# Kernel optimization log

Measured on AMD Instinct MI355X. Metric: run time of the kernel, lower is better.

The kernel has to match this reference:

```python
import jax, jax.numpy as jnp
import numpy as np

TOP_K = 2
ALPHA = 1.702
LIMIT = 7.0


def setup_inputs() -> dict:
    key = jax.random.key(0)
    ks = jax.random.split(key, 7)
    B, S, H, I, E = 1, 2048, 1024, 1024, 8
    scale = 0.02
    return {
        "hidden_states": jax.random.normal(ks[0], (B, S, H), dtype=jnp.float32),
        "router_w": jax.random.normal(ks[1], (H, E), dtype=jnp.float32) * scale,
        "router_b": jax.random.normal(ks[2], (E,), dtype=jnp.float32) * scale,
        "gate_up_proj": jax.random.normal(ks[3], (E, H, 2 * I), dtype=jnp.float32) * scale,
        "gate_up_bias": jax.random.normal(ks[4], (E, 2 * I), dtype=jnp.float32) * scale,
        "down_proj": jax.random.normal(ks[5], (E, I, H), dtype=jnp.float32) * scale,
        "down_bias": jax.random.normal(ks[6], (E, H), dtype=jnp.float32) * scale,
    }


def reference(hidden_states, router_w, router_b, gate_up_proj, gate_up_bias, down_proj, down_bias):
    # hidden_states: [B, S, H]; gate_up_proj: [E, H, 2I]; down_proj: [E, I, H]
    E = gate_up_proj.shape[0]
    # --- router (GPT-OSS style): top-k logits, softmax over top-k, scatter to E slots ---
    logits = jnp.einsum("bsh,he->bse", hidden_states, router_w) + router_b  # [B,S,E]
    top_vals, top_idx = jax.lax.top_k(logits, TOP_K)                         # [B,S,K]
    topk_weights = jax.nn.softmax(top_vals, axis=-1)                         # [B,S,K]
    onehot = jax.nn.one_hot(top_idx, E, dtype=logits.dtype)                  # [B,S,K,E]
    router_scores = jnp.einsum("bsk,bske->bse", topk_weights, onehot)        # [B,S,E]
    # --- expert compute (dense over the small expert axis; selection via gather below,
    #     which matches the sparsity-masked grouped matmul + all_to_all_combine math) ---
    gu = jnp.einsum("bsh,ehf->bsef", hidden_states, gate_up_proj) + gate_up_bias  # [B,S,E,2I]
    gate = gu[..., 0::2]  # interleaved gate
    up = gu[..., 1::2]    # interleaved up
    gate = jnp.minimum(gate, LIMIT)
    up = jnp.maximum(jnp.minimum(up, LIMIT), -LIMIT)
    glu = gate * jax.nn.sigmoid(gate * ALPHA)
    activated = (up + 1.0) * glu                                             # [B,S,E,I]
    down = jnp.einsum("bsei,eih->bseh", activated, down_proj) + down_bias    # [B,S,E,H]
    # combine: gather each token's K selected expert outputs, weighted sum
    sel = jnp.take_along_axis(down, top_idx[..., None], axis=2)              # [B,S,K,H]
    output = jnp.einsum("bskh,bsk->bsh", sel, topk_weights)                  # [B,S,H]
    return output, router_scores
```

## Files before the change

kernel.cpp:

```cpp
#include <hip/hip_runtime.h>
#include <stdint.h>


#define Sd 2048
#define Hd 1024
#define Id 1024

typedef __bf16 bf16x8 __attribute__((ext_vector_type(8)));
typedef _Float16 f16x8 __attribute__((ext_vector_type(8)));
typedef float f32x4 __attribute__((ext_vector_type(4)));

__device__ __forceinline__ f32x4 mfma_bf16(bf16x8 a, bf16x8 b, f32x4 c) {
  return __builtin_amdgcn_mfma_f32_16x16x32_bf16(a, b, c, 0, 0, 0);
}

__device__ __forceinline__ void gload16(const __bf16* g, __bf16* l) {
  __builtin_amdgcn_global_load_lds(
      (const __attribute__((address_space(1))) unsigned int*)g,
      (__attribute__((address_space(3))) unsigned int*)l, 16, 0, 0);
}

__device__ __forceinline__ unsigned int packbf(float lo, float hi) {
  __bf16 a = (__bf16)lo, b = (__bf16)hi;
  return (unsigned int)__builtin_bit_cast(unsigned short, a) |
         ((unsigned int)__builtin_bit_cast(unsigned short, b) << 16);
}

__global__ __launch_bounds__(256) void k_router(
    const float* __restrict__ x, const float* __restrict__ rw,
    const float* __restrict__ rb, float* __restrict__ scores,
    float* __restrict__ topw, int* __restrict__ eid,
    __bf16* __restrict__ xb) {
  const int lane = threadIdx.x & 63;
  const int t = blockIdx.x * 4 + (threadIdx.x >> 6);
  float acc[8];
#pragma unroll
  for (int e = 0; e < 8; ++e) acc[e] = 0.f;
  const float* xr = x + (size_t)t * Hd;
  unsigned int* xbo = (unsigned int*)(xb + (size_t)t * Hd);
#pragma unroll
  for (int j = 0; j < 8; ++j) {
    int h = j * 128 + lane * 2;
    float2 xv = *(const float2*)(xr + h);
    xbo[h >> 1] = packbf(xv.x, xv.y);
    const float4* wp = (const float4*)(rw + h * 8);
    float4 a0 = wp[0], a1 = wp[1], b0 = wp[2], b1 = wp[3];
    acc[0] += xv.x * a0.x; acc[1] += xv.x * a0.y;
    acc[2] += xv.x * a0.z; acc[3] += xv.x * a0.w;
    acc[4] += xv.x * a1.x; acc[5] += xv.x * a1.y;
    acc[6] += xv.x * a1.z; acc[7] += xv.x * a1.w;
    acc[0] += xv.y * b0.x; acc[1] += xv.y * b0.y;
    acc[2] += xv.y * b0.z; acc[3] += xv.y * b0.w;
    acc[4] += xv.y * b1.x; acc[5] += xv.y * b1.y;
    acc[6] += xv.y * b1.z; acc[7] += xv.y * b1.w;
  }
#pragma unroll
  for (int m = 32; m >= 1; m >>= 1) {
#pragma unroll
    for (int e = 0; e < 8; ++e) acc[e] += __shfl_xor(acc[e], m, 64);
  }
  if (lane == 0) {
    float lg[8];
#pragma unroll
    for (int e = 0; e < 8; ++e) lg[e] = acc[e] + rb[e];
    int i0 = 0; float v0 = lg[0];
#pragma unroll
    for (int e = 1; e < 8; ++e) if (lg[e] > v0) { v0 = lg[e]; i0 = e; }
    int i1 = -1; float v1 = -3.4e38f;
#pragma unroll
    for (int e = 0; e < 8; ++e) if (e != i0 && lg[e] > v1) { v1 = lg[e]; i1 = e; }
    float e1 = __expf(v1 - v0);
    float s = 1.f + e1;
    float w0 = 1.f / s, w1v = e1 / s;
#pragma unroll
    for (int e = 0; e < 8; ++e)
      scores[t * 8 + e] = (e == i0) ? w0 : ((e == i1) ? w1v : 0.f);
    topw[t * 2] = w0;
    topw[t * 2 + 1] = w1v;
    eid[t] = i0 | (i1 << 4);
  }
}

__global__ __launch_bounds__(256) void k_assign(
    const int* __restrict__ eid, int* __restrict__ cnt,
    int* __restrict__ assign, int* __restrict__ tokmap) {
  __shared__ int lcnt[8];
  const int tid = threadIdx.x;
  if (tid < 8) lcnt[tid] = 0;
  __syncthreads();
  for (int t = tid; t < 2048; t += 256) {
    int v = eid[t];
    int i0 = v & 15, i1 = v >> 4;
    int s0 = atomicAdd(&lcnt[i0], 1);
    assign[i0 * 2048 + s0] = t * 2;
    tokmap[t * 2] = (i0 << 11) | s0;
    int s1 = atomicAdd(&lcnt[i1], 1);
    assign[i1 * 2048 + s1] = t * 2 + 1;
    tokmap[t * 2 + 1] = (i1 << 11) | s1;
  }
  __syncthreads();
  if (tid < 8) cnt[tid] = lcnt[tid];
}

__global__ __launch_bounds__(256) void k_gather(
    const __bf16* __restrict__ xb, const int* __restrict__ cnt,
    const int* __restrict__ assign, __bf16* __restrict__ xg) {
  const int u = blockIdx.x;
  int acc = 0, myE = -1, myU0 = 0, nE = 0;
#pragma unroll
  for (int q = 0; q < 8; ++q) {
    int units = ((cnt[q] + 255) >> 8) * 16;
    if (u >= acc && u < acc + units) { myE = q; myU0 = acc; nE = cnt[q]; }
    acc += units;
  }
  if (myE < 0) return;
  const int lane = threadIdx.x & 63;
  const int wv = threadIdx.x >> 6;
  const int row = lane & 15, koff = (lane >> 4) * 8;
  const int slot = (u - myU0) * 16 + row;
  const bool valid = slot < nE;
  int tok = 0;
  if (valid) tok = assign[myE * 2048 + slot] >> 1;
  const __bf16* src = xb + (size_t)tok * Hd + koff;
#pragma unroll
  for (int s = 0; s < 8; ++s) {
    int k32 = wv + 4 * s;
    bf16x8 v;
#pragma unroll
    for (int j = 0; j < 8; ++j) v[j] = (__bf16)0.f;
    if (valid) v = *(const bf16x8*)(src + k32 * 32);
    *(bf16x8*)(xg + (((size_t)u * 32 + k32) * 64 + lane) * 8) = v;
  }
}

__global__ __launch_bounds__(256) void k_pre1(const float* __restrict__ wgu,
                                              __bf16* __restrict__ w1f) {
  const int b = blockIdx.x;
  const int nt = b & 7, kt = (b >> 3) & 15, e = b >> 7;
  __shared__ unsigned int Ls[16][16][34];
  const int tid = threadIdx.x;
  const int w = tid >> 6, lane = tid & 63;
  const float* src = wgu + (size_t)e * (1024 * 2048) +
                     (size_t)(kt * 64 + w * 16) * 2048 + nt * 256;
  const int i0 = lane * 2;
  const int c0 = i0 & 15, u0 = (i0 >> 4) * 2;
  const int c1 = (i0 + 1) & 15, u1 = ((i0 + 1) >> 4) * 2;
#pragma unroll
  for (int rp = 0; rp < 8; ++rp) {
    float4 fa = *(const float4*)(src + (size_t)(rp * 2) * 2048 + lane * 4);
    float4 fb = *(const float4*)(src + (size_t)(rp * 2 + 1) * 2048 + lane * 4);
    int r = w * 8 + rp;
    Ls[u0][c0][r] = packbf(fa.x, fb.x);
    Ls[u0 + 1][c0][r] = packbf(fa.y, fb.y);
    Ls[u1][c1][r] = packbf(fa.z, fb.z);
    Ls[u1 + 1][c1][r] = packbf(fa.w, fb.w);
  }
  __syncthreads();
  const int khi = lane >> 4, c = lane & 15;
#pragma unroll
  for (int uu = 0; uu < 8; ++uu) {
    int ul = w * 8 + uu, vu = ul >> 1, k32l = ul & 1;
    const unsigned int* p = &Ls[vu][c][k32l * 16 + khi * 4];
    uint2 q0 = *(const uint2*)p;
    uint2 q1 = *(const uint2*)(p + 2);
    int itg = nt * 8 + (vu >> 1), vf = vu & 1;
    size_t row = ((size_t)(e * 64 + itg) * 2 + vf) * 32 + (kt * 2 + k32l);
    uint4 o = {q0.x, q0.y, q1.x, q1.y};
    *(uint4*)(w1f + row * 512 + lane * 8) = o;
  }
}

__global__ __launch_bounds__(256) void k_pre2(const float* __restrict__ wdn,
                                              __bf16* __restrict__ w2f) {
  const int b = blockIdx.x;
  const int nt = b & 3, kt = (b >> 2) & 15, e = b >> 6;
  __shared__ unsigned int Ls[16][16][34];
  const int tid = threadIdx.x;
  const int w = tid >> 6, lane = tid & 63;
  const float* src = wdn + (size_t)e * (1024 * 1024) +
                     (size_t)(kt * 64 + w * 16) * 1024 + nt * 256;
#pragma unroll
  for (int rp = 0; rp < 8; ++rp) {
    float4 fa = *(const float4*)(src + (size_t)(rp * 2) * 1024 + lane * 4);
    float4 fb = *(const float4*)(src + (size_t)(rp * 2 + 1) * 1024 + lane * 4);
    int r = w * 8 + rp;
    float va[4] = {fa.x, fa.y, fa.z, fa.w};
    float vb[4] = {fb.x, fb.y, fb.z, fb.w};
#pragma unroll
    for (int q = 0; q < 4; ++q) {
      int cl = lane * 4 + q;
      Ls[cl >> 4][cl & 15][r] = packbf(va[q], vb[q]);
    }
  }
  __syncthreads();
  const int khi = lane >> 4, c = lane & 15;
#pragma unroll
  for (int uu = 0; uu < 8; ++uu) {
    int ul = w * 8 + uu, Fl = ul >> 1, k32l = ul & 1;
    const unsigned int* p = &Ls[Fl][c][k32l * 16 + khi * 4];
    uint2 q0 = *(const uint2*)p;
    uint2 q1 = *(const uint2*)(p + 2);
    size_t row = (size_t)(e * 64 + nt * 16 + Fl) * 32 + (kt * 2 + k32l);
    uint4 o = {q0.x, q0.y, q1.x, q1.y};
    *(uint4*)(w2f + row * 512 + lane * 8) = o;
  }
}

__global__ __launch_bounds__(512, 2) void k_gemm1(
    const __bf16* __restrict__ xg, const __bf16* __restrict__ w1f,
    const float* __restrict__ gub, const int* __restrict__ cnt,
    __bf16* __restrict__ abuf) {
  const int e = blockIdx.x & 7;
  const int r = blockIdx.x >> 3;
  const int it = r & 31;
  const int ms = r >> 5;
  const int n = cnt[e];
  if (n <= 0) return;
  __shared__ __align__(16) __bf16 Bs[4][32][512];
  __shared__ __align__(16) __bf16 Ts[256][48];
  const int tid = threadIdx.x;
  const int lane = tid & 63;
  const int wv = tid >> 6;

#pragma unroll
  for (int s = 0; s < 16; ++s) {
    int idx = s * 512 + tid;
    int v = idx >> 11, k = (idx >> 6) & 31, l = idx & 63;
    size_t rowv = (size_t)(e * 64 + it * 2 + (v >> 1)) * 2 + (v & 1);
    gload16(w1f + (rowv * 32 + k) * 512 + l * 8, &Bs[v][k][l * 8]);
  }
  float bgv[2], buv[2];
#pragma unroll
  for (int p = 0; p < 2; ++p) {
    const int col = it * 32 + p * 16 + (lane & 15);
    bgv[p] = gub[e * 2048 + 2 * col];
    buv[p] = gub[e * 2048 + 2 * col + 1];
  }
  int eb = 0;
#pragma unroll
  for (int q = 0; q < 8; ++q) eb += (q < e) ? (((cnt[q] + 255) >> 8) << 8) : 0;
  const int u0 = eb >> 4;
  const int nmt = (n + 255) >> 8;

  for (int mt = ms; mt < nmt; mt += 2) {
    __syncthreads();
    const __bf16* ap0 =
        xg + ((size_t)(u0 + mt * 16 + 2 * wv) * 32) * 512 + lane * 8;
    const __bf16* ap1 = ap0 + (size_t)32 * 512;
    f32x4 acc[2][4];
#pragma unroll
    for (int a = 0; a < 2; ++a)
#pragma unroll
      for (int b = 0; b < 4; ++b) acc[a][b] = (f32x4){0.f, 0.f, 0.f, 0.f};
    bf16x8 pf[4][2];
#pragma unroll
    for (int d = 0; d < 4; ++d) {
      pf[d][0] = *(const bf16x8*)(ap0 + d * 512);
      pf[d][1] = *(const bf16x8*)(ap1 + d * 512);
    }
#pragma unroll 4
    for (int ks = 0; ks < 28; ++ks) {
      bf16x8 b[4];
#pragma unroll
      for (int v = 0; v < 4; ++v) b[v] = *(const bf16x8*)&Bs[v][ks][lane * 8];
#pragma unroll
      for (int v = 0; v < 4; ++v) {
        acc[0][v] = mfma_bf16(pf[ks & 3][0], b[v], acc[0][v]);
        acc[1][v] = mfma_bf16(pf[ks & 3][1], b[v], acc[1][v]);
      }
      pf[ks & 3][0] = *(const bf16x8*)(ap0 + (ks + 4) * 512);
      pf[ks & 3][1] = *(const bf16x8*)(ap1 + (ks + 4) * 512);
    }
#pragma unroll
    for (int ks = 28; ks < 32; ++ks) {
      bf16x8 b[4];
#pragma unroll
      for (int v = 0; v < 4; ++v) b[v] = *(const bf16x8*)&Bs[v][ks][lane * 8];
#pragma unroll
      for (int v = 0; v < 4; ++v) {
        acc[0][v] = mfma_bf16(pf[ks & 3][0], b[v], acc[0][v]);
        acc[1][v] = mfma_bf16(pf[ks & 3][1], b[v], acc[1][v]);
      }
    }
#pragma unroll
    for (int itgl = 0; itgl < 2; ++itgl) {
      const int colL = itgl * 16 + (lane & 15);
#pragma unroll
      for (int mi = 0; mi < 2; ++mi) {
        f32x4 ag = acc[mi][itgl * 2];
        f32x4 au = acc[mi][itgl * 2 + 1];
#pragma unroll
        for (int rr = 0; rr < 4; ++rr) {
          int row = wv * 32 + mi * 16 + (lane >> 4) * 4 + rr;
          float g = fminf(ag[rr] + bgv[itgl], 7.f);
          float u = fminf(fmaxf(au[rr] + buv[itgl], -7.f), 7.f);
          float sg = 1.f / (1.f + __expf(-1.702f * g));
          Ts[row][colL] = (__bf16)((u + 1.f) * (g * sg));
        }
      }
    }
    __syncthreads();
#pragma unroll
    for (int h2 = 0; h2 < 2; ++h2) {
      int idx = h2 * 512 + tid;
      int sbl = idx >> 6, l = idx & 63;
      bf16x8 v = *(const bf16x8*)&Ts[sbl * 16 + (l & 15)][(l >> 4) * 8];
      size_t o = ((size_t)(u0 + mt * 16 + sbl) * 32 + it) * 512 + l * 8;
      *(bf16x8*)(abuf + o) = v;
    }
  }
}

__global__ __launch_bounds__(512, 2) void k_gemm2(
    const __bf16* __restrict__ abuf, const __bf16* __restrict__ w2f,
    const float* __restrict__ dnb, const int* __restrict__ cnt,
    const int* __restrict__ assign, const float* __restrict__ topw,
    _Float16* __restrict__ dbuf) {
  const int e = blockIdx.x & 7;
  const int r = blockIdx.x >> 3;
  const int ht = r & 15;
  const int ms = r >> 4;
  const int n = cnt[e];
  if (n <= 0) return;
  __shared__ __align__(16) __bf16 Bs[4][32][512];
  __shared__ float wgt[256];
  const int tid = threadIdx.x;
  const int lane = tid & 63;
  const int wv = tid >> 6;

#pragma unroll
  for (int s = 0; s < 16; ++s) {
    int idx = s * 512 + tid;
    int v = idx >> 11, k = (idx >> 6) & 31, l = idx & 63;
    size_t rowv = (size_t)(e * 64 + ht * 4 + v);
    gload16(w2f + (rowv * 32 + k) * 512 + l * 8, &Bs[v][k][l * 8]);
  }
  int eb = 0;
#pragma unroll
  for (int q = 0; q < 8; ++q) eb += (q < e) ? (((cnt[q] + 255) >> 8) << 8) : 0;
  const int u0 = eb >> 4;
  const int nmt = (n + 255) >> 8;

  for (int mt = ms; mt < nmt; mt += 4) {
    __syncthreads();
    if (tid < 256) {
      int slot = mt * 256 + tid;
      int en = (slot < n) ? assign[e * 2048 + slot] : -1;
      wgt[tid] = (en >= 0) ? topw[en] : 0.f;
    }
    __syncthreads();
    const __bf16* ab0 =
        abuf + ((size_t)(u0 + mt * 16 + 2 * wv) * 32) * 512 + lane * 8;
    const __bf16* ab1 = ab0 + (size_t)32 * 512;
    f32x4 acc[2][4];
#pragma unroll
    for (int a = 0; a < 2; ++a)
#pragma unroll
      for (int b = 0; b < 4; ++b) acc[a][b] = (f32x4){0.f, 0.f, 0.f, 0.f};
    bf16x8 pf[4][2];
#pragma unroll
    for (int d = 0; d < 4; ++d) {
      pf[d][0] = *(const bf16x8*)(ab0 + d * 512);
      pf[d][1] = *(const bf16x8*)(ab1 + d * 512);
    }
#pragma unroll 4
    for (int ks = 0; ks < 28; ++ks) {
      bf16x8 b[4];
#pragma unroll
      for (int v = 0; v < 4; ++v) b[v] = *(const bf16x8*)&Bs[v][ks][lane * 8];
#pragma unroll
      for (int v = 0; v < 4; ++v) {
        acc[0][v] = mfma_bf16(pf[ks & 3][0], b[v], acc[0][v]);
        acc[1][v] = mfma_bf16(pf[ks & 3][1], b[v], acc[1][v]);
      }
      pf[ks & 3][0] = *(const bf16x8*)(ab0 + (ks + 4) * 512);
      pf[ks & 3][1] = *(const bf16x8*)(ab1 + (ks + 4) * 512);
    }
#pragma unroll
    for (int ks = 28; ks < 32; ++ks) {
      bf16x8 b[4];
#pragma unroll
      for (int v = 0; v < 4; ++v) b[v] = *(const bf16x8*)&Bs[v][ks][lane * 8];
#pragma unroll
      for (int v = 0; v < 4; ++v) {
        acc[0][v] = mfma_bf16(pf[ks & 3][0], b[v], acc[0][v]);
        acc[1][v] = mfma_bf16(pf[ks & 3][1], b[v], acc[1][v]);
      }
    }
#pragma unroll
    for (int v = 0; v < 4; ++v) {
      const int nn = ht * 64 + v * 16 + (lane & 15);
      const float bias = dnb[e * 1024 + nn];
#pragma unroll
      for (int mi = 0; mi < 2; ++mi) {
#pragma unroll
        for (int rr = 0; rr < 4; ++rr) {
          int row = wv * 32 + mi * 16 + (lane >> 4) * 4 + rr;
          int slot = eb + mt * 256 + row;
          dbuf[(size_t)slot * 1024 + nn] =
              (_Float16)(wgt[row] * (acc[mi][v][rr] + bias));
        }
      }
    }
  }
}

__global__ __launch_bounds__(256) void k_combine(
    const _Float16* __restrict__ dbuf, const int* __restrict__ tokmap,
    const int* __restrict__ cnt, float* __restrict__ out) {
  const int t = blockIdx.x * 4 + (threadIdx.x >> 6);
  const int lane = threadIdx.x & 63;
  int v0 = tokmap[t * 2], v1 = tokmap[t * 2 + 1];
  int e0 = v0 >> 11, e1 = v1 >> 11;
  int b0 = 0, b1 = 0, acc = 0;
#pragma unroll
  for (int q = 0; q < 8; ++q) {
    if (q == e0) b0 = acc;
    if (q == e1) b1 = acc;
    acc += ((cnt[q] + 255) >> 8) << 8;
  }
  const _Float16* r0 = dbuf + (size_t)(b0 + (v0 & 2047)) * 1024 + lane * 16;
  const _Float16* r1 = dbuf + (size_t)(b1 + (v1 & 2047)) * 1024 + lane * 16;
  float* o = out + (size_t)t * 1024 + lane * 16;
#pragma unroll
  for (int h = 0; h < 2; ++h) {
    f16x8 a = *(const f16x8*)(r0 + h * 8);
    f16x8 b = *(const f16x8*)(r1 + h * 8);
    float4 o0, o1;
    o0.x = (float)a[0] + (float)b[0];
    o0.y = (float)a[1] + (float)b[1];
    o0.z = (float)a[2] + (float)b[2];
    o0.w = (float)a[3] + (float)b[3];
    o1.x = (float)a[4] + (float)b[4];
    o1.y = (float)a[5] + (float)b[5];
    o1.z = (float)a[6] + (float)b[6];
    o1.w = (float)a[7] + (float)b[7];
    *(float4*)(o + h * 8) = o0;
    *(float4*)(o + h * 8 + 4) = o1;
  }
}

extern "C" void kernel_launch(void* const* d_in, const int* in_sizes, int n_in,
                              void* d_out, int out_size, void* d_ws, size_t ws_size,
                              hipStream_t stream) {
  const float* x   = (const float*)d_in[0];
  const float* rw  = (const float*)d_in[1];
  const float* rb  = (const float*)d_in[2];
  const float* wgu = (const float*)d_in[3];
  const float* gub = (const float*)d_in[4];
  const float* wdn = (const float*)d_in[5];
  const float* dnb = (const float*)d_in[6];
  float* out = (float*)d_out;
  float* scores = out + (size_t)Sd * Hd;

  char* ws = (char*)d_ws;
  int* cnt     = (int*)ws;
  int* assign  = (int*)(ws + 256);
  float* topw  = (float*)(ws + 256 + 65536);
  int* tokmap  = (int*)(ws + 256 + 65536 + 16384);
  int* eid     = (int*)(ws + 256 + 65536 + 32768);
  __bf16* xg   = (__bf16*)(ws + ((size_t)1 << 20));
  __bf16* abuf = (__bf16*)(ws + ((size_t)15 << 20));
  __bf16* xb   = (__bf16*)(ws + ((size_t)28 << 20));
  __bf16* w1f  = (__bf16*)(ws + ((size_t)28 << 20));
  __bf16* w2f  = (__bf16*)(ws + ((size_t)28 << 20));
  _Float16* dbuf = (_Float16*)(ws + ((size_t)44 << 20));

  k_router<<<512, 256, 0, stream>>>(x, rw, rb, scores, topw, eid, xb);
  k_assign<<<1, 256, 0, stream>>>(eid, cnt, assign, tokmap);
  k_gather<<<384, 256, 0, stream>>>(xb, cnt, assign, xg);
  k_pre1<<<1024, 256, 0, stream>>>(wgu, w1f);
  k_gemm1<<<512, 512, 0, stream>>>(xg, w1f, gub, cnt, abuf);
  k_pre2<<<512, 256, 0, stream>>>(wdn, w2f);
  k_gemm2<<<512, 512, 0, stream>>>(abuf, w2f, dnb, cnt, assign, topw, dbuf);
  k_combine<<<512, 256, 0, stream>>>(dbuf, tokmap, cnt, out);
}
```

Baseline: 114.2 us.

## Merge router and weight-prepack kernels into one launch and skip idle GEMM blocks

Combines the router, gate_up weight repack and down weight repack into a single kernel that dispatches on block index, removing two launches and letting the independent conversions run concurrently. This required giving w1f and w2f their own workspace regions instead of aliasing xb, so all three buffers now coexist. The GEMM kernels now exit early for blocks whose M-slice exceeds the expert's tile count, before issuing weight loads into LDS. The fused kernel carries the LDS array for every block, including the router blocks that do not use it.

```diff
diff --git a/kernel.cpp b/kernel.cpp
--- a/kernel.cpp
+++ b/kernel.cpp
@@ -26,58 +26,127 @@
          ((unsigned int)__builtin_bit_cast(unsigned short, b) << 16);
 }
 
-__global__ __launch_bounds__(256) void k_router(
+__global__ __launch_bounds__(256) void k_prep(
     const float* __restrict__ x, const float* __restrict__ rw,
     const float* __restrict__ rb, float* __restrict__ scores,
-    float* __restrict__ topw, int* __restrict__ eid,
-    __bf16* __restrict__ xb) {
-  const int lane = threadIdx.x & 63;
-  const int t = blockIdx.x * 4 + (threadIdx.x >> 6);
-  float acc[8];
-#pragma unroll
-  for (int e = 0; e < 8; ++e) acc[e] = 0.f;
-  const float* xr = x + (size_t)t * Hd;
-  unsigned int* xbo = (unsigned int*)(xb + (size_t)t * Hd);
-#pragma unroll
-  for (int j = 0; j < 8; ++j) {
-    int h = j * 128 + lane * 2;
-    float2 xv = *(const float2*)(xr + h);
-    xbo[h >> 1] = packbf(xv.x, xv.y);
-    const float4* wp = (const float4*)(rw + h * 8);
-    float4 a0 = wp[0], a1 = wp[1], b0 = wp[2], b1 = wp[3];
-    acc[0] += xv.x * a0.x; acc[1] += xv.x * a0.y;
-    acc[2] += xv.x * a0.z; acc[3] += xv.x * a0.w;
-    acc[4] += xv.x * a1.x; acc[5] += xv.x * a1.y;
-    acc[6] += xv.x * a1.z; acc[7] += xv.x * a1.w;
-    acc[0] += xv.y * b0.x; acc[1] += xv.y * b0.y;
-    acc[2] += xv.y * b0.z; acc[3] += xv.y * b0.w;
-    acc[4] += xv.y * b1.x; acc[5] += xv.y * b1.y;
-    acc[6] += xv.y * b1.z; acc[7] += xv.y * b1.w;
-  }
-#pragma unroll
-  for (int m = 32; m >= 1; m >>= 1) {
-#pragma unroll
-    for (int e = 0; e < 8; ++e) acc[e] += __shfl_xor(acc[e], m, 64);
-  }
-  if (lane == 0) {
-    float lg[8];
-#pragma unroll
-    for (int e = 0; e < 8; ++e) lg[e] = acc[e] + rb[e];
-    int i0 = 0; float v0 = lg[0];
-#pragma unroll
-    for (int e = 1; e < 8; ++e) if (lg[e] > v0) { v0 = lg[e]; i0 = e; }
-    int i1 = -1; float v1 = -3.4e38f;
-#pragma unroll
-    for (int e = 0; e < 8; ++e) if (e != i0 && lg[e] > v1) { v1 = lg[e]; i1 = e; }
-    float e1 = __expf(v1 - v0);
-    float s = 1.f + e1;
-    float w0 = 1.f / s, w1v = e1 / s;
-#pragma unroll
-    for (int e = 0; e < 8; ++e)
-      scores[t * 8 + e] = (e == i0) ? w0 : ((e == i1) ? w1v : 0.f);
-    topw[t * 2] = w0;
-    topw[t * 2 + 1] = w1v;
-    eid[t] = i0 | (i1 << 4);
+    float* __restrict__ topw, int* __restrict__ eid, __bf16* __restrict__ xb,
+    const float* __restrict__ wgu, __bf16* __restrict__ w1f,
+    const float* __restrict__ wdn, __bf16* __restrict__ w2f) {
+  __shared__ unsigned int Ls[16][16][34];
+  const int blk = blockIdx.x;
+  const int tid = threadIdx.x;
+  const int lane = tid & 63;
+  if (blk < 512) {
+    const int t = blk * 4 + (tid >> 6);
+    float acc[8];
+#pragma unroll
+    for (int e = 0; e < 8; ++e) acc[e] = 0.f;
+    const float* xr = x + (size_t)t * Hd;
+    unsigned int* xbo = (unsigned int*)(xb + (size_t)t * Hd);
+#pragma unroll
+    for (int j = 0; j < 8; ++j) {
+      int h = j * 128 + lane * 2;
+      float2 xv = *(const float2*)(xr + h);
+      xbo[h >> 1] = packbf(xv.x, xv.y);
+      const float4* wp = (const float4*)(rw + h * 8);
+      float4 a0 = wp[0], a1 = wp[1], b0 = wp[2], b1 = wp[3];
+      acc[0] += xv.x * a0.x; acc[1] += xv.x * a0.y;
+      acc[2] += xv.x * a0.z; acc[3] += xv.x * a0.w;
+      acc[4] += xv.x * a1.x; acc[5] += xv.x * a1.y;
+      acc[6] += xv.x * a1.z; acc[7] += xv.x * a1.w;
+      acc[0] += xv.y * b0.x; acc[1] += xv.y * b0.y;
+      acc[2] += xv.y * b0.z; acc[3] += xv.y * b0.w;
+      acc[4] += xv.y * b1.x; acc[5] += xv.y * b1.y;
+      acc[6] += xv.y * b1.z; acc[7] += xv.y * b1.w;
+    }
+#pragma unroll
+    for (int m = 32; m >= 1; m >>= 1) {
+#pragma unroll
+      for (int e = 0; e < 8; ++e) acc[e] += __shfl_xor(acc[e], m, 64);
+    }
+    if (lane == 0) {
+      float lg[8];
+#pragma unroll
+      for (int e = 0; e < 8; ++e) lg[e] = acc[e] + rb[e];
+      int i0 = 0; float v0 = lg[0];
+#pragma unroll
+      for (int e = 1; e < 8; ++e) if (lg[e] > v0) { v0 = lg[e]; i0 = e; }
+      int i1 = -1; float v1 = -3.4e38f;
+#pragma unroll
+      for (int e = 0; e < 8; ++e) if (e != i0 && lg[e] > v1) { v1 = lg[e]; i1 = e; }
+      float e1 = __expf(v1 - v0);
+      float s = 1.f + e1;
+      float w0 = 1.f / s, w1v = e1 / s;
+#pragma unroll
+      for (int e = 0; e < 8; ++e)
+        scores[t * 8 + e] = (e == i0) ? w0 : ((e == i1) ? w1v : 0.f);
+      topw[t * 2] = w0;
+      topw[t * 2 + 1] = w1v;
+      eid[t] = i0 | (i1 << 4);
+    }
+  } else if (blk < 1536) {
+    const int b = blk - 512;
+    const int nt = b & 7, kt = (b >> 3) & 15, e = b >> 7;
+    const int w = tid >> 6;
+    const float* src = wgu + (size_t)e * (1024 * 2048) +
+                       (size_t)(kt * 64 + w * 16) * 2048 + nt * 256;
+    const int i0 = lane * 2;
+    const int c0 = i0 & 15, u0 = (i0 >> 4) * 2;
+    const int c1 = (i0 + 1) & 15, u1 = ((i0 + 1) >> 4) * 2;
+#pragma unroll
+    for (int rp = 0; rp < 8; ++rp) {
+      float4 fa = *(const float4*)(src + (size_t)(rp * 2) * 2048 + lane * 4);
+      float4 fb = *(const float4*)(src + (size_t)(rp * 2 + 1) * 2048 + lane * 4);
+      int r = w * 8 + rp;
+      Ls[u0][c0][r] = packbf(fa.x, fb.x);
+      Ls[u0 + 1][c0][r] = packbf(fa.y, fb.y);
+      Ls[u1][c1][r] = packbf(fa.z, fb.z);
+      Ls[u1 + 1][c1][r] = packbf(fa.w, fb.w);
+    }
+    __syncthreads();
+    const int khi = lane >> 4, c = lane & 15;
+#pragma unroll
+    for (int uu = 0; uu < 8; ++uu) {
+      int ul = w * 8 + uu, vu = ul >> 1, k32l = ul & 1;
+      const unsigned int* p = &Ls[vu][c][k32l * 16 + khi * 4];
+      uint2 q0 = *(const uint2*)p;
+      uint2 q1 = *(const uint2*)(p + 2);
+      int itg = nt * 8 + (vu >> 1), vf = vu & 1;
+      size_t row = ((size_t)(e * 64 + itg) * 2 + vf) * 32 + (kt * 2 + k32l);
+      uint4 o = {q0.x, q0.y, q1.x, q1.y};
+      *(uint4*)(w1f + row * 512 + lane * 8) = o;
+    }
+  } else {
+    const int b = blk - 1536;
+    const int nt = b & 3, kt = (b >> 2) & 15, e = b >> 6;
+    const int w = tid >> 6;
+    const float* src = wdn + (size_t)e * (1024 * 1024) +
+                       (size_t)(kt * 64 + w * 16) * 1024 + nt * 256;
+#pragma unroll
+    for (int rp = 0; rp < 8; ++rp) {
+      float4 fa = *(const float4*)(src + (size_t)(rp * 2) * 1024 + lane * 4);
+      float4 fb = *(const float4*)(src + (size_t)(rp * 2 + 1) * 1024 + lane * 4);
+      int r = w * 8 + rp;
+      float va[4] = {fa.x, fa.y, fa.z, fa.w};
+      float vb[4] = {fb.x, fb.y, fb.z, fb.w};
+#pragma unroll
+      for (int q = 0; q < 4; ++q) {
+        int cl = lane * 4 + q;
+        Ls[cl >> 4][cl & 15][r] = packbf(va[q], vb[q]);
+      }
+    }
+    __syncthreads();
+    const int khi = lane >> 4, c = lane & 15;
+#pragma unroll
+    for (int uu = 0; uu < 8; ++uu) {
+      int ul = w * 8 + uu, Fl = ul >> 1, k32l = ul & 1;
+      const unsigned int* p = &Ls[Fl][c][k32l * 16 + khi * 4];
+      uint2 q0 = *(const uint2*)p;
+      uint2 q1 = *(const uint2*)(p + 2);
+      size_t row = (size_t)(e * 64 + nt * 16 + Fl) * 32 + (kt * 2 + k32l);
+      uint4 o = {q0.x, q0.y, q1.x, q1.y};
+      *(uint4*)(w2f + row * 512 + lane * 8) = o;
+    }
   }
 }
 
@@ -133,79 +202,6 @@
   }
 }
 
-__global__ __launch_bounds__(256) void k_pre1(const float* __restrict__ wgu,
-                                              __bf16* __restrict__ w1f) {
-  const int b = blockIdx.x;
-  const int nt = b & 7, kt = (b >> 3) & 15, e = b >> 7;
-  __shared__ unsigned int Ls[16][16][34];
-  const int tid = threadIdx.x;
-  const int w = tid >> 6, lane = tid & 63;
-  const float* src = wgu + (size_t)e * (1024 * 2048) +
-                     (size_t)(kt * 64 + w * 16) * 2048 + nt * 256;
-  const int i0 = lane * 2;
-  const int c0 = i0 & 15, u0 = (i0 >> 4) * 2;
-  const int c1 = (i0 + 1) & 15, u1 = ((i0 + 1) >> 4) * 2;
-#pragma unroll
-  for (int rp = 0; rp < 8; ++rp) {
-    float4 fa = *(const float4*)(src + (size_t)(rp * 2) * 2048 + lane * 4);
-    float4 fb = *(const float4*)(src + (size_t)(rp * 2 + 1) * 2048 + lane * 4);
-    int r = w * 8 + rp;
-    Ls[u0][c0][r] = packbf(fa.x, fb.x);
-    Ls[u0 + 1][c0][r] = packbf(fa.y, fb.y);
-    Ls[u1][c1][r] = packbf(fa.z, fb.z);
-    Ls[u1 + 1][c1][r] = packbf(fa.w, fb.w);
-  }
-  __syncthreads();
-  const int khi = lane >> 4, c = lane & 15;
-#pragma unroll
-  for (int uu = 0; uu < 8; ++uu) {
-    int ul = w * 8 + uu, vu = ul >> 1, k32l = ul & 1;
-    const unsigned int* p = &Ls[vu][c][k32l * 16 + khi * 4];
-    uint2 q0 = *(const uint2*)p;
-    uint2 q1 = *(const uint2*)(p + 2);
-    int itg = nt * 8 + (vu >> 1), vf = vu & 1;
-    size_t row = ((size_t)(e * 64 + itg) * 2 + vf) * 32 + (kt * 2 + k32l);
-    uint4 o = {q0.x, q0.y, q1.x, q1.y};
-    *(uint4*)(w1f + row * 512 + lane * 8) = o;
-  }
-}
-
-__global__ __launch_bounds__(256) void k_pre2(const float* __restrict__ wdn,
-                                              __bf16* __restrict__ w2f) {
-  const int b = blockIdx.x;
-  const int nt = b & 3, kt = (b >> 2) & 15, e = b >> 6;
-  __shared__ unsigned int Ls[16][16][34];
-  const int tid = threadIdx.x;
-  const int w = tid >> 6, lane = tid & 63;
-  const float* src = wdn + (size_t)e * (1024 * 1024) +
-                     (size_t)(kt * 64 + w * 16) * 1024 + nt * 256;
-#pragma unroll
-  for (int rp = 0; rp < 8; ++rp) {
-    float4 fa = *(const float4*)(src + (size_t)(rp * 2) * 1024 + lane * 4);
-    float4 fb = *(const float4*)(src + (size_t)(rp * 2 + 1) * 1024 + lane * 4);
-    int r = w * 8 + rp;
-    float va[4] = {fa.x, fa.y, fa.z, fa.w};
-    float vb[4] = {fb.x, fb.y, fb.z, fb.w};
-#pragma unroll
-    for (int q = 0; q < 4; ++q) {
-      int cl = lane * 4 + q;
-      Ls[cl >> 4][cl & 15][r] = packbf(va[q], vb[q]);
-    }
-  }
-  __syncthreads();
-  const int khi = lane >> 4, c = lane & 15;
-#pragma unroll
-  for (int uu = 0; uu < 8; ++uu) {
-    int ul = w * 8 + uu, Fl = ul >> 1, k32l = ul & 1;
-    const unsigned int* p = &Ls[Fl][c][k32l * 16 + khi * 4];
-    uint2 q0 = *(const uint2*)p;
-    uint2 q1 = *(const uint2*)(p + 2);
-    size_t row = (size_t)(e * 64 + nt * 16 + Fl) * 32 + (kt * 2 + k32l);
-    uint4 o = {q0.x, q0.y, q1.x, q1.y};
-    *(uint4*)(w2f + row * 512 + lane * 8) = o;
-  }
-}
-
 __global__ __launch_bounds__(512, 2) void k_gemm1(
     const __bf16* __restrict__ xg, const __bf16* __restrict__ w1f,
     const float* __restrict__ gub, const int* __restrict__ cnt,
@@ -216,6 +212,8 @@
   const int ms = r >> 5;
   const int n = cnt[e];
   if (n <= 0) return;
+  const int nmt = (n + 255) >> 8;
+  if (ms >= nmt) return;
   __shared__ __align__(16) __bf16 Bs[4][32][512];
   __shared__ __align__(16) __bf16 Ts[256][48];
   const int tid = threadIdx.x;
@@ -240,7 +238,6 @@
 #pragma unroll
   for (int q = 0; q < 8; ++q) eb += (q < e) ? (((cnt[q] + 255) >> 8) << 8) : 0;
   const int u0 = eb >> 4;
-  const int nmt = (n + 255) >> 8;
 
   for (int mt = ms; mt < nmt; mt += 2) {
     __syncthreads();
@@ -322,6 +319,8 @@
   const int ms = r >> 4;
   const int n = cnt[e];
   if (n <= 0) return;
+  const int nmt = (n + 255) >> 8;
+  if (ms >= nmt) return;
   __shared__ __align__(16) __bf16 Bs[4][32][512];
   __shared__ float wgt[256];
   const int tid = threadIdx.x;
@@ -339,7 +338,6 @@
 #pragma unroll
   for (int q = 0; q < 8; ++q) eb += (q < e) ? (((cnt[q] + 255) >> 8) << 8) : 0;
   const int u0 = eb >> 4;
-  const int nmt = (n + 255) >> 8;
 
   for (int mt = ms; mt < nmt; mt += 4) {
     __syncthreads();
@@ -462,16 +460,15 @@
   __bf16* xg   = (__bf16*)(ws + ((size_t)1 << 20));
   __bf16* abuf = (__bf16*)(ws + ((size_t)15 << 20));
   __bf16* xb   = (__bf16*)(ws + ((size_t)28 << 20));
-  __bf16* w1f  = (__bf16*)(ws + ((size_t)28 << 20));
-  __bf16* w2f  = (__bf16*)(ws + ((size_t)28 << 20));
-  _Float16* dbuf = (_Float16*)(ws + ((size_t)44 << 20));
-
-  k_router<<<512, 256, 0, stream>>>(x, rw, rb, scores, topw, eid, xb);
+  __bf16* w1f  = (__bf16*)(ws + ((size_t)33 << 20));
+  __bf16* w2f  = (__bf16*)(ws + ((size_t)66 << 20));
+  _Float16* dbuf = (_Float16*)(ws + ((size_t)83 << 20));
+
+  k_prep<<<2048, 256, 0, stream>>>(x, rw, rb, scores, topw, eid, xb,
+                                   wgu, w1f, wdn, w2f);
   k_assign<<<1, 256, 0, stream>>>(eid, cnt, assign, tokmap);
   k_gather<<<384, 256, 0, stream>>>(xb, cnt, assign, xg);
-  k_pre1<<<1024, 256, 0, stream>>>(wgu, w1f);
   k_gemm1<<<512, 512, 0, stream>>>(xg, w1f, gub, cnt, abuf);
-  k_pre2<<<512, 256, 0, stream>>>(wdn, w2f);
   k_gemm2<<<512, 512, 0, stream>>>(abuf, w2f, dnb, cnt, assign, topw, dbuf);
   k_combine<<<512, 256, 0, stream>>>(dbuf, tokmap, cnt, out);
 }
```

Result: faster. 102.0 us (-10.7%).
